# Optimization experiments

Hardware: AMD Instinct MI355X
Metric: run time of the kernel (lower is better)

The kernel has to match this reference:

```python
import jax, jax.numpy as jnp
import numpy as np

EPS = 1e-12  # torch F.normalize eps

def _l2norm(x):
    # matches torch.nn.functional.normalize(x, dim=-1): x / max(||x||, eps)
    n = jnp.sqrt(jnp.sum(x * x, axis=-1, keepdims=True))
    return x / jnp.maximum(n, EPS)

def setup_inputs() -> dict:
    key = jax.random.key(0)
    k1, k2, k3 = jax.random.split(key, 3)
    N, D, H, C = 4096, 16384, 256, 28
    return {
        "features": jax.random.normal(k1, (N, H), dtype=jnp.float32),
        "ex_features": jax.random.normal(k2, (D, H), dtype=jnp.float32),
        "ex_class_reps": jax.random.normal(k3, (D, C), dtype=jnp.float32),
        "p_factor": 3,
    }

def reference(features, ex_features, ex_class_reps, p_factor):
    # cosine similarity: [N, D]
    s = _l2norm(features) @ _l2norm(ex_features).T
    # power-law activation preserving sign
    a = jnp.sign(s) * jnp.abs(s) ** p_factor
    intensity = a.sum(axis=1)           # [N]
    echo = a @ ex_class_reps            # [N, C]
    return (echo, intensity)
```

## Files before the change

kernel.cpp:

```cpp
#include <hip/hip_runtime.h>
#include <cstdint>

#define HDIM 256
#define MT   256
#define BD   32
#define SPLITS 32

typedef short bf16x8 __attribute__((ext_vector_type(8)));
typedef short bf16x4 __attribute__((ext_vector_type(4)));
typedef float f32x4  __attribute__((ext_vector_type(4)));

typedef const __attribute__((address_space(1))) short as1_short;
typedef __attribute__((address_space(3))) short as3_short;

static __device__ __forceinline__ short f2bf(float x) {
    union { float f; uint32_t u; } v; v.f = x;
    uint32_t u = v.u;
    uint32_t r = (u + 0x7fffu + ((u >> 16) & 1u)) >> 16;
    return (short)r;
}

__global__ __launch_bounds__(256) void prep_kernel(const float* __restrict__ fsrc,
                                                   const float* __restrict__ esrc,
                                                   const float* __restrict__ reps,
                                                   short* __restrict__ dst,
                                                   short* __restrict__ rt,
                                                   int N, int rows_total,
                                                   int D, int C, int nb_nrm) {
    __shared__ float lds[128][29];
    const int tid = threadIdx.x;
    if ((int)blockIdx.x < nb_nrm) {
        int wv = tid >> 6;
        int lane = tid & 63;
        int row = blockIdx.x * 4 + wv;
        if (row >= rows_total) return;
        const float* src = (row < N) ? (fsrc + (size_t)row * HDIM)
                                     : (esrc + (size_t)(row - N) * HDIM);
        const float4 v = *(const float4*)(src + lane * 4);
        float ss = v.x * v.x + v.y * v.y + v.z * v.z + v.w * v.w;
        #pragma unroll
        for (int m = 1; m < 64; m <<= 1) ss += __shfl_xor(ss, m, 64);
        float scale = 1.0f / fmaxf(sqrtf(ss), 1e-12f);
        short4 o;
        o.x = f2bf(v.x * scale); o.y = f2bf(v.y * scale);
        o.z = f2bf(v.z * scale); o.w = f2bf(v.w * scale);
        int chunk = (lane >> 1) ^ (row & 7);
        *(short4*)(dst + (size_t)row * HDIM + chunk * 8 + (lane & 1) * 4) = o;
    } else {
        const int bx = blockIdx.x - nb_nrm;
        const int d0 = bx * 128;
        const int total = 128 * C;
        const float* src = reps + (size_t)d0 * C;
        for (int i = tid; i < total; i += 256)
            lds[i / C][i % C] = src[i];
        __syncthreads();
        const int c = tid >> 3;
        const int dsub = (tid & 7) * 16;
        short* dstp = rt + (size_t)c * D + d0 + dsub;
        #pragma unroll
        for (int j0 = 0; j0 < 16; j0 += 4) {
            short4 o;
            float v0, v1, v2, v3;
            if (c < C) {
                v0 = lds[dsub + j0 + 0][c]; v1 = lds[dsub + j0 + 1][c];
                v2 = lds[dsub + j0 + 2][c]; v3 = lds[dsub + j0 + 3][c];
            } else {
                float f = (c == C) ? 1.0f : 0.0f;
                v0 = v1 = v2 = v3 = f;
            }
            o.x = f2bf(v0); o.y = f2bf(v1); o.z = f2bf(v2); o.w = f2bf(v3);
            *(short4*)(dstp + j0) = o;
        }
    }
}

__global__ __launch_bounds__(256, 2) void fused_kernel(const short* __restrict__ Fn,
                                                       const short* __restrict__ En,
                                                       const short* __restrict__ Rt,
                                                       const int* __restrict__ pptr,
                                                       float* __restrict__ partial,
                                                       int N, int D, int C, int Dchunk) {
    __shared__ __align__(16) short lds_en[2][BD * HDIM];

    const int tid  = threadIdx.x;
    const int lane = tid & 63;
    const int wv   = tid >> 6;
    const int q    = lane >> 4;
    const int l    = lane & 15;
    const int p    = pptr[0];

    const int Mbase = blockIdx.y * MT;
    const int dbase = blockIdx.x * Dchunk;

    const f32x4 zf = {0.0f, 0.0f, 0.0f, 0.0f};

    bf16x8 afrag[4][8];
    #pragma unroll
    for (int fn = 0; fn < 4; ++fn) {
        const short* rowp = Fn + (size_t)(Mbase + wv * 64 + fn * 16 + l) * HDIM;
        #pragma unroll
        for (int ks = 0; ks < 8; ++ks)
            afrag[fn][ks] = *(const bf16x8*)(rowp + (((ks * 4 + q) ^ (l & 7)) << 3));
    }

    f32x4 echo_acc[4][2];
    #pragma unroll
    for (int fn = 0; fn < 4; ++fn) { echo_acc[fn][0] = zf; echo_acc[fn][1] = zf; }

    const int iters = Dchunk / BD;

    #define STAGE(buf_, it_)                                                        \
        {                                                                           \
            const short* gbase = En + (size_t)(dbase + (it_) * BD) * HDIM + tid * 8;\
            _Pragma("unroll")                                                       \
            for (int i = 0; i < 4; ++i) {                                           \
                as3_short* lp = (as3_short*)(lds_en[buf_] + (i * 256 + wv * 64) * 8);\
                __builtin_amdgcn_global_load_lds((as1_short*)(gbase + i * 2048),    \
                                                 lp, 16, 0, 0);                     \
            }                                                                       \
        }

    STAGE(0, 0)

    const short* rtp = Rt + (size_t)l * D + q * 4;

    for (int it = 0; it < iters; ++it) {
        const int buf = it & 1;
        __syncthreads();
        if (it + 1 < iters) STAGE(buf ^ 1, it + 1)

        const int d0 = dbase + it * BD;

        f32x4 sT[2][4];
        #pragma unroll
        for (int en = 0; en < 2; ++en)
            #pragma unroll
            for (int fn = 0; fn < 4; ++fn) sT[en][fn] = zf;
        #pragma unroll
        for (int ks = 0; ks < 8; ++ks) {
            #pragma unroll
            for (int en = 0; en < 2; ++en) {
                const int row  = en * 16 + l;
                const int slot = (ks * 4 + q) ^ (l & 7);
                bf16x8 ef = *(const bf16x8*)(lds_en[buf] + row * HDIM + slot * 8);
                #pragma unroll
                for (int fn = 0; fn < 4; ++fn)
                    sT[en][fn] = __builtin_amdgcn_mfma_f32_16x16x32_bf16(ef, afrag[fn][ks], sT[en][fn], 0, 0, 0);
            }
        }

        bf16x4 pfrag[4][2];
        #pragma unroll
        for (int en = 0; en < 2; ++en) {
            #pragma unroll
            for (int fn = 0; fn < 4; ++fn) {
                bf16x4 pf;
                #pragma unroll
                for (int r = 0; r < 4; ++r) {
                    float sv = sT[en][fn][r];
                    float a;
                    if (p == 3)      a = sv * sv * sv;
                    else if (p == 1) a = sv;
                    else if (p == 2) a = sv * fabsf(sv);
                    else             a = copysignf(powf(fabsf(sv), (float)p), sv);
                    pf[r] = f2bf(a);
                }
                pfrag[fn][en] = pf;
            }
        }

        #pragma unroll
        for (int dblk = 0; dblk < 2; ++dblk) {
            const int doff = d0 + dblk * 16;
            bf16x4 rt0 = *(const bf16x4*)(rtp + doff);
            bf16x4 rt1 = *(const bf16x4*)(rtp + (size_t)16 * D + doff);
            #pragma unroll
            for (int fn = 0; fn < 4; ++fn) {
                echo_acc[fn][0] = __builtin_amdgcn_mfma_f32_16x16x16bf16_1k(rt0, pfrag[fn][dblk], echo_acc[fn][0], 0, 0, 0);
                echo_acc[fn][1] = __builtin_amdgcn_mfma_f32_16x16x16bf16_1k(rt1, pfrag[fn][dblk], echo_acc[fn][1], 0, 0, 0);
            }
        }
    }

    #pragma unroll
    for (int fn = 0; fn < 4; ++fn) {
        const int grow = Mbase + wv * 64 + fn * 16 + l;
        float* rowp = partial + ((size_t)blockIdx.x * N + grow) * 32 + q * 4;
        *(f32x4*)(rowp)      = echo_acc[fn][0];
        *(f32x4*)(rowp + 16) = echo_acc[fn][1];
    }

    #undef STAGE
}

__global__ __launch_bounds__(256) void reduce_kernel(const float* __restrict__ partial,
                                                     float* __restrict__ echo,
                                                     float* __restrict__ inten,
                                                     int N, int splits, int C) {
    int t = blockIdx.x * 256 + threadIdx.x;
    int row = t >> 5, c = t & 31;
    if (row >= N || c > C) return;
    float s = 0.0f;
    for (int k = 0; k < splits; ++k)
        s += partial[((size_t)k * N + (size_t)row) * 32 + c];
    if (c < C) echo[(size_t)row * C + c] = s;
    else       inten[row] = s;
}

extern "C" void kernel_launch(void* const* d_in, const int* in_sizes, int n_in,
                              void* d_out, int out_size, void* d_ws, size_t ws_size,
                              hipStream_t stream) {
    const int N = in_sizes[0] / HDIM;
    const int D = in_sizes[1] / HDIM;
    const int C = in_sizes[2] / D;

    const float* feat = (const float*)d_in[0];
    const float* exf  = (const float*)d_in[1];
    const float* reps = (const float*)d_in[2];
    const int*   p    = (const int*)d_in[3];

    short* Fn = (short*)d_ws;
    short* En = Fn + (size_t)N * HDIM;
    short* Rt = En + (size_t)D * HDIM;
    float* partial = (float*)(Rt + (size_t)32 * D);

    float* echo  = (float*)d_out;
    float* inten = echo + (size_t)N * C;

    const int nb_nrm = (N + D) / 4;
    hipLaunchKernelGGL(prep_kernel, dim3(nb_nrm + D / 128), dim3(256), 0, stream,
                       feat, exf, reps, Fn, Rt, N, N + D, D, C, nb_nrm);

    const int Dchunk = D / SPLITS;
    hipLaunchKernelGGL(fused_kernel, dim3(SPLITS, N / MT), dim3(256), 0, stream,
                       Fn, En, Rt, p, partial, N, D, C, Dchunk);

    hipLaunchKernelGGL(reduce_kernel, dim3(N * 32 / 256), dim3(256), 0, stream,
                       partial, echo, inten, N, SPLITS, C);
}
```

Before: 144.3 us.

## Give each wave its own LDS staging buffers and drop block-wide barriers

The fused kernel now gives each wave a private double-buffered LDS region holding a 16-row window of the ex_features tile. Each wave loads its own window through global_load_lds and waits with vmcnt/lgkmcnt instead of __syncthreads, prefetching two windows ahead. The intent is to remove block-wide barrier stalls and let waves run independently. In exchange, every wave fetches the same E tile separately, which multiplies global/L2 traffic by four and leaves less MFMA work per window. The prep kernel also now normalizes 16 rows per block instead of 4, cutting the block count.

```diff
diff --git a/kernel.cpp b/kernel.cpp
--- a/kernel.cpp
+++ b/kernel.cpp
@@ -3,8 +3,9 @@
 
 #define HDIM 256
 #define MT   256
-#define BD   32
+#define BDW  16
 #define SPLITS 32
+#define RPB  16
 
 typedef short bf16x8 __attribute__((ext_vector_type(8)));
 typedef short bf16x4 __attribute__((ext_vector_type(4)));
@@ -32,20 +33,24 @@
     if ((int)blockIdx.x < nb_nrm) {
         int wv = tid >> 6;
         int lane = tid & 63;
-        int row = blockIdx.x * 4 + wv;
-        if (row >= rows_total) return;
-        const float* src = (row < N) ? (fsrc + (size_t)row * HDIM)
-                                     : (esrc + (size_t)(row - N) * HDIM);
-        const float4 v = *(const float4*)(src + lane * 4);
-        float ss = v.x * v.x + v.y * v.y + v.z * v.z + v.w * v.w;
-        #pragma unroll
-        for (int m = 1; m < 64; m <<= 1) ss += __shfl_xor(ss, m, 64);
-        float scale = 1.0f / fmaxf(sqrtf(ss), 1e-12f);
-        short4 o;
-        o.x = f2bf(v.x * scale); o.y = f2bf(v.y * scale);
-        o.z = f2bf(v.z * scale); o.w = f2bf(v.w * scale);
-        int chunk = (lane >> 1) ^ (row & 7);
-        *(short4*)(dst + (size_t)row * HDIM + chunk * 8 + (lane & 1) * 4) = o;
+        int row0 = blockIdx.x * RPB + wv * 4;
+        #pragma unroll
+        for (int rr = 0; rr < 4; ++rr) {
+            int row = row0 + rr;
+            if (row >= rows_total) continue;
+            const float* src = (row < N) ? (fsrc + (size_t)row * HDIM)
+                                         : (esrc + (size_t)(row - N) * HDIM);
+            const float4 v = *(const float4*)(src + lane * 4);
+            float ss = v.x * v.x + v.y * v.y + v.z * v.z + v.w * v.w;
+            #pragma unroll
+            for (int m = 1; m < 64; m <<= 1) ss += __shfl_xor(ss, m, 64);
+            float scale = 1.0f / fmaxf(sqrtf(ss), 1e-12f);
+            short4 o;
+            o.x = f2bf(v.x * scale); o.y = f2bf(v.y * scale);
+            o.z = f2bf(v.z * scale); o.w = f2bf(v.w * scale);
+            int chunk = (lane >> 1) ^ (row & 7);
+            *(short4*)(dst + (size_t)row * HDIM + chunk * 8 + (lane & 1) * 4) = o;
+        }
     } else {
         const int bx = blockIdx.x - nb_nrm;
         const int d0 = bx * 128;
@@ -80,7 +85,7 @@
                                                        const int* __restrict__ pptr,
                                                        float* __restrict__ partial,
                                                        int N, int D, int C, int Dchunk) {
-    __shared__ __align__(16) short lds_en[2][BD * HDIM];
+    __shared__ __align__(16) short lds_en[4][2][BDW * HDIM];
 
     const int tid  = threadIdx.x;
     const int lane = tid & 63;
@@ -107,78 +112,75 @@
     #pragma unroll
     for (int fn = 0; fn < 4; ++fn) { echo_acc[fn][0] = zf; echo_acc[fn][1] = zf; }
 
-    const int iters = Dchunk / BD;
-
-    #define STAGE(buf_, it_)                                                        \
+    const int nwin = Dchunk / BDW;
+
+    #define STAGE_W(buf_, it_)                                                      \
         {                                                                           \
-            const short* gbase = En + (size_t)(dbase + (it_) * BD) * HDIM + tid * 8;\
+            const short* gbase = En + (size_t)(dbase + (it_) * BDW) * HDIM + lane * 8;\
+            as3_short* lbase = (as3_short*)(&lds_en[wv][buf_][0]);                  \
             _Pragma("unroll")                                                       \
-            for (int i = 0; i < 4; ++i) {                                           \
-                as3_short* lp = (as3_short*)(lds_en[buf_] + (i * 256 + wv * 64) * 8);\
-                __builtin_amdgcn_global_load_lds((as1_short*)(gbase + i * 2048),    \
-                                                 lp, 16, 0, 0);                     \
+            for (int i = 0; i < 8; ++i) {                                           \
+                __builtin_amdgcn_global_load_lds((as1_short*)(gbase + i * 512),     \
+                                                 lbase + i * 512, 16, 0, 0);        \
             }                                                                       \
         }
 
-    STAGE(0, 0)
-
     const short* rtp = Rt + (size_t)l * D + q * 4;
 
-    for (int it = 0; it < iters; ++it) {
+    STAGE_W(0, 0)
+    STAGE_W(1, 1)
+
+    for (int it = 0; it < nwin; ++it) {
         const int buf = it & 1;
-        __syncthreads();
-        if (it + 1 < iters) STAGE(buf ^ 1, it + 1)
-
-        const int d0 = dbase + it * BD;
-
-        f32x4 sT[2][4];
-        #pragma unroll
-        for (int en = 0; en < 2; ++en)
+
+        if (it < nwin - 1) {
+            asm volatile("s_waitcnt vmcnt(8)" ::: "memory");
+        } else {
+            asm volatile("s_waitcnt vmcnt(0)" ::: "memory");
+        }
+        __builtin_amdgcn_sched_barrier(0);
+
+        const int d0 = dbase + it * BDW;
+
+        f32x4 sT[4];
+        #pragma unroll
+        for (int fn = 0; fn < 4; ++fn) sT[fn] = zf;
+        #pragma unroll
+        for (int ks = 0; ks < 8; ++ks) {
+            const int slot = (ks * 4 + q) ^ (l & 7);
+            bf16x8 ef = *(const bf16x8*)(&lds_en[wv][buf][l * HDIM + slot * 8]);
             #pragma unroll
-            for (int fn = 0; fn < 4; ++fn) sT[en][fn] = zf;
-        #pragma unroll
-        for (int ks = 0; ks < 8; ++ks) {
+            for (int fn = 0; fn < 4; ++fn)
+                sT[fn] = __builtin_amdgcn_mfma_f32_16x16x32_bf16(ef, afrag[fn][ks], sT[fn], 0, 0, 0);
+        }
+
+        asm volatile("s_waitcnt lgkmcnt(0)" ::: "memory");
+        __builtin_amdgcn_sched_barrier(0);
+        if (it + 2 < nwin) STAGE_W(buf, it + 2)
+
+        bf16x4 pfrag[4];
+        #pragma unroll
+        for (int fn = 0; fn < 4; ++fn) {
+            bf16x4 pf;
             #pragma unroll
-            for (int en = 0; en < 2; ++en) {
-                const int row  = en * 16 + l;
-                const int slot = (ks * 4 + q) ^ (l & 7);
-                bf16x8 ef = *(const bf16x8*)(lds_en[buf] + row * HDIM + slot * 8);
-                #pragma unroll
-                for (int fn = 0; fn < 4; ++fn)
-                    sT[en][fn] = __builtin_amdgcn_mfma_f32_16x16x32_bf16(ef, afrag[fn][ks], sT[en][fn], 0, 0, 0);
+            for (int r = 0; r < 4; ++r) {
+                float sv = sT[fn][r];
+                float a;
+                if (p == 3)      a = sv * sv * sv;
+                else if (p == 1) a = sv;
+                else if (p == 2) a = sv * fabsf(sv);
+                else             a = copysignf(powf(fabsf(sv), (float)p), sv);
+                pf[r] = f2bf(a);
             }
-        }
-
-        bf16x4 pfrag[4][2];
-        #pragma unroll
-        for (int en = 0; en < 2; ++en) {
-            #pragma unroll
-            for (int fn = 0; fn < 4; ++fn) {
-                bf16x4 pf;
-                #pragma unroll
-                for (int r = 0; r < 4; ++r) {
-                    float sv = sT[en][fn][r];
-                    float a;
-                    if (p == 3)      a = sv * sv * sv;
-                    else if (p == 1) a = sv;
-                    else if (p == 2) a = sv * fabsf(sv);
-                    else             a = copysignf(powf(fabsf(sv), (float)p), sv);
-                    pf[r] = f2bf(a);
-                }
-                pfrag[fn][en] = pf;
-            }
-        }
-
-        #pragma unroll
-        for (int dblk = 0; dblk < 2; ++dblk) {
-            const int doff = d0 + dblk * 16;
-            bf16x4 rt0 = *(const bf16x4*)(rtp + doff);
-            bf16x4 rt1 = *(const bf16x4*)(rtp + (size_t)16 * D + doff);
-            #pragma unroll
-            for (int fn = 0; fn < 4; ++fn) {
-                echo_acc[fn][0] = __builtin_amdgcn_mfma_f32_16x16x16bf16_1k(rt0, pfrag[fn][dblk], echo_acc[fn][0], 0, 0, 0);
-                echo_acc[fn][1] = __builtin_amdgcn_mfma_f32_16x16x16bf16_1k(rt1, pfrag[fn][dblk], echo_acc[fn][1], 0, 0, 0);
-            }
+            pfrag[fn] = pf;
+        }
+
+        bf16x4 rt0 = *(const bf16x4*)(rtp + d0);
+        bf16x4 rt1 = *(const bf16x4*)(rtp + (size_t)16 * D + d0);
+        #pragma unroll
+        for (int fn = 0; fn < 4; ++fn) {
+            echo_acc[fn][0] = __builtin_amdgcn_mfma_f32_16x16x16bf16_1k(rt0, pfrag[fn], echo_acc[fn][0], 0, 0, 0);
+            echo_acc[fn][1] = __builtin_amdgcn_mfma_f32_16x16x16bf16_1k(rt1, pfrag[fn], echo_acc[fn][1], 0, 0, 0);
         }
     }
 
@@ -190,7 +192,7 @@
         *(f32x4*)(rowp + 16) = echo_acc[fn][1];
     }
 
-    #undef STAGE
+    #undef STAGE_W
 }
 
 __global__ __launch_bounds__(256) void reduce_kernel(const float* __restrict__ partial,
@@ -227,7 +229,7 @@
     float* echo  = (float*)d_out;
     float* inten = echo + (size_t)N * C;
 
-    const int nb_nrm = (N + D) / 4;
+    const int nb_nrm = (N + D + RPB - 1) / RPB;
     hipLaunchKernelGGL(prep_kernel, dim3(nb_nrm + D / 128), dim3(256), 0, stream,
                        feat, exf, reps, Fn, Rt, N, N + D, D, C, nb_nrm);
 
```

Result: no change. 143.0 us (-0.9%).
